# Performance work log

Hardware: AMD Instinct MI355X
Metric: run time of the kernel (lower is better)

Reference implementation:

```python
import jax, jax.numpy as jnp
import numpy as np

NUM_NODES = 116
EMBED = 64
HIDDEN = 64
OUT_FEAT = 116


def mish(x):
    return x * jnp.tanh(jax.nn.softplus(x))


def sage_conv(x, src, dst, w_l, b_l, w_r, n):
    # PyG SAGEConv (mean aggr): out = lin_l(mean_{j->i} x_j) + lin_r(x_i)
    agg = jax.ops.segment_sum(x[src], dst, num_segments=n)
    cnt = jax.ops.segment_sum(jnp.ones((src.shape[0],), x.dtype), dst, num_segments=n)
    mean = agg / jnp.clip(cnt, 1.0)[:, None]
    return mean @ w_l.T + b_l + x @ w_r.T


def setup_inputs() -> dict:
    key = jax.random.key(0)
    ks = jax.random.split(key, 12)
    B = 64
    N = B * NUM_NODES          # 7424 total nodes
    E = N * 32                 # 237568 edges
    d_in = EMBED * NUM_NODES   # 7424
    d_hid = HIDDEN * NUM_NODES # 7424
    d_out = OUT_FEAT * NUM_NODES  # 13456

    def lin_w(k, fan_out, fan_in):
        s = 1.0 / np.sqrt(fan_in)
        return jax.random.uniform(k, (fan_out, fan_in), jnp.float32, -s, s)

    return {
        "z": jax.random.normal(ks[0], (N, EMBED), jnp.float32),
        "edge_index": jax.random.randint(ks[1], (2, E), 0, N, jnp.int64),
        "batch_size": B,
        "w1_l": lin_w(ks[2], EMBED, EMBED),
        "b1_l": jnp.zeros((EMBED,), jnp.float32),
        "w1_r": lin_w(ks[3], EMBED, EMBED),
        "w2_l": lin_w(ks[4], EMBED, EMBED),
        "b2_l": jnp.zeros((EMBED,), jnp.float32),
        "w2_r": lin_w(ks[5], EMBED, EMBED),
        "fc1_w": lin_w(ks[6], d_hid, d_in),
        "fc1_b": jax.random.uniform(ks[7], (d_hid,), jnp.float32, -1/np.sqrt(d_in), 1/np.sqrt(d_in)),
        "fc2_w": lin_w(ks[8], d_out, d_hid),
        "fc2_b": jax.random.uniform(ks[9], (d_out,), jnp.float32, -1/np.sqrt(d_hid), 1/np.sqrt(d_hid)),
    }


def reference(z, edge_index, batch_size, w1_l, b1_l, w1_r, w2_l, b2_l, w2_r,
              fc1_w, fc1_b, fc2_w, fc2_b):
    n = z.shape[0]
    src, dst = edge_index[0], edge_index[1]
    h = mish(sage_conv(z, src, dst, w1_l, b1_l, w1_r, n))
    h = mish(sage_conv(h, src, dst, w2_l, b2_l, w2_r, n))
    h_flat = h.reshape(batch_size, NUM_NODES * EMBED)
    hidden = mish(h_flat @ fc1_w.T + fc1_b)
    x_rec = (hidden @ fc2_w.T + fc2_b).reshape(batch_size, NUM_NODES, OUT_FEAT)
    # enforce symmetry, unit diagonal
    sym = 0.5 * (x_rec + jnp.swapaxes(x_rec, 1, 2))
    eye = jnp.eye(NUM_NODES, dtype=bool)[None]
    sym = jnp.where(eye, jnp.asarray(1.0, sym.dtype), sym)
    return sym.reshape(batch_size * NUM_NODES, OUT_FEAT)
```

## Files before the change

### kernel.cpp

```cpp
#include <hip/hip_runtime.h>
#include <math.h>

#define NODES_TOT 7424
#define EDGES     237568
#define BATCH     64
#define NN        116
#define KDIM      7424
#define N1        7424
#define N2        13456
#define NKB       116
#define KSPLIT1   16
#define KSPLIT2   8

typedef __attribute__((ext_vector_type(8))) short bf16x8;
typedef __attribute__((ext_vector_type(4))) float f32x4;
typedef __attribute__((ext_vector_type(4))) short s16x4;

__device__ __forceinline__ float mish_f(float v) {
    float sp = fmaxf(v, 0.0f) + log1pf(expf(-fabsf(v)));
    return v * tanhf(sp);
}

__device__ __forceinline__ unsigned short bf_rne(float f) {
    unsigned u = __float_as_uint(f);
    u += 0x7fffu + ((u >> 16) & 1u);
    return (unsigned short)(u >> 16);
}

__global__ void zero_kernel(int* __restrict__ p, int n) {
    int i = blockIdx.x * 256 + threadIdx.x;
    if (i < n) p[i] = 0;
}

__global__ void hist_kernel(const int* __restrict__ dst, int* __restrict__ hist) {
    int e = blockIdx.x * 256 + threadIdx.x;
    if (e < EDGES) atomicAdd(&hist[dst[e]], 1);
}

__global__ void scan_kernel(const int* __restrict__ hist, int* __restrict__ row_start,
                            int* __restrict__ cursor) {
    __shared__ int s[1024];
    int t = threadIdx.x;
    int base = t * 8;
    int loc[8];
    int sum = 0;
    #pragma unroll
    for (int c = 0; c < 8; ++c) {
        int idx = base + c;
        int v = (idx < NODES_TOT) ? hist[idx] : 0;
        loc[c] = sum;
        sum += v;
    }
    s[t] = sum;
    __syncthreads();
    for (int off = 1; off < 1024; off <<= 1) {
        int v = (t >= off) ? s[t - off] : 0;
        __syncthreads();
        s[t] += v;
        __syncthreads();
    }
    int excl = s[t] - sum;
    #pragma unroll
    for (int c = 0; c < 8; ++c) {
        int idx = base + c;
        if (idx < NODES_TOT) {
            int r = excl + loc[c];
            row_start[idx] = r;
            cursor[idx] = r;
        }
    }
}

__global__ void csr_fill_kernel(const int* __restrict__ src, const int* __restrict__ dst,
                                int* __restrict__ cursor, int* __restrict__ csr_src) {
    int e = blockIdx.x * 256 + threadIdx.x;
    if (e < EDGES) {
        int p = atomicAdd(&cursor[dst[e]], 1);
        csr_src[p] = src[e];
    }
}

template <bool BF>
__global__ void __launch_bounds__(256) conv_kernel(
        const float* __restrict__ x, const int* __restrict__ csr_src,
        const int* __restrict__ row_start, const int* __restrict__ deg_arr,
        const float* __restrict__ w_l, const float* __restrict__ b_l,
        const float* __restrict__ w_r, void* __restrict__ h_out_v) {
    __shared__ float wlT[64 * 64];
    __shared__ float wrT[64 * 64];
    __shared__ float mv[4][64];
    __shared__ float xv[4][64];
    int t = threadIdx.x;
    for (int i = 0; i < 16; ++i) {
        int idx = t + i * 256;
        int f = idx >> 6, k = idx & 63;
        wlT[k * 64 + f] = w_l[idx];
        wrT[k * 64 + f] = w_r[idx];
    }
    int g = t >> 6, f = t & 63;
    __syncthreads();
    for (int nb = blockIdx.x * 4; nb < NODES_TOT; nb += gridDim.x * 4) {
        int node = nb + g;
        int deg = deg_arr[node];
        int rs = row_start[node];
        float sum = 0.f;
        for (int e = 0; e < deg; ++e) {
            int s = csr_src[rs + e];
            sum += x[s * 64 + f];
        }
        float mean = sum / (float)max(deg, 1);
        mv[g][f] = mean;
        xv[g][f] = x[node * 64 + f];
        __syncthreads();
        float o = b_l[f];
        #pragma unroll
        for (int k = 0; k < 64; ++k) {
            o = fmaf(mv[g][k], wlT[k * 64 + f], o);
            o = fmaf(xv[g][k], wrT[k * 64 + f], o);
        }
        float m = mish_f(o);
        if (BF) ((unsigned short*)h_out_v)[node * 64 + f] = bf_rne(m);
        else    ((float*)h_out_v)[node * 64 + f] = m;
        __syncthreads();
    }
}

template <int KSHIFT>
__global__ void __launch_bounds__(256) gemm_tile(
        const unsigned short* __restrict__ Abf, const float* __restrict__ W,
        float* __restrict__ Cp, int N) {
    __shared__ __align__(16) short Wsh[512 * 8];
    int t = threadIdx.x;
    int bx = blockIdx.x, by = blockIdx.y;
    int kb0 = (by * NKB) >> KSHIFT;
    int kb1 = ((by + 1) * NKB) >> KSHIFT;
    int n0 = bx * 64;
    int r = t >> 2, q = t & 3;
    int wr = n0 + r; if (wr >= N) wr = N - 1;
    const float* wsrc = W + (size_t)wr * KDIM + q * 4;
    int half = q & 1;
    int fbase = q >> 1;
    int wv = t >> 6, l = t & 63, l15 = l & 15, hi = l >> 4;
    f32x4 acc[4];
    #pragma unroll
    for (int g = 0; g < 4; ++g) acc[g] = (f32x4){0.f, 0.f, 0.f, 0.f};

    f32x4 w[4];
    {
        size_t k0 = (size_t)kb0 * 64;
        #pragma unroll
        for (int i = 0; i < 4; ++i) w[i] = *(const f32x4*)(wsrc + k0 + i * 16);
    }
    for (int kb = kb0; kb < kb1; ++kb) {
        s16x4 cv[4];
        #pragma unroll
        for (int i = 0; i < 4; ++i)
            #pragma unroll
            for (int j = 0; j < 4; ++j) cv[i][j] = (short)bf_rne(w[i][j]);
        __syncthreads();
        #pragma unroll
        for (int i = 0; i < 4; ++i)
            *(s16x4*)&Wsh[((i * 2 + fbase) * 64 + r) * 8 + half * 4] = cv[i];
        __syncthreads();
        if (kb + 1 < kb1) {
            size_t kn = (size_t)(kb + 1) * 64;
            #pragma unroll
            for (int i = 0; i < 4; ++i) w[i] = *(const f32x4*)(wsrc + kn + i * 16);
        }
        size_t k0 = (size_t)kb * 64;
        #pragma unroll
        for (int s = 0; s < 2; ++s) {
            int fw = s * 4 + hi;
            bf16x8 bh = *(const bf16x8*)&Wsh[(fw * 64 + wv * 16 + l15) * 8];
            #pragma unroll
            for (int g = 0; g < 4; ++g) {
                bf16x8 av = *(const bf16x8*)(Abf + (size_t)(g * 16 + l15) * KDIM + k0 + fw * 8);
                acc[g] = __builtin_amdgcn_mfma_f32_16x16x32_bf16(av, bh, acc[g], 0, 0, 0);
            }
        }
    }
    int gn = n0 + wv * 16 + l15;
    if (gn < N) {
        float* cp = Cp + (size_t)by * 64 * N;
        #pragma unroll
        for (int g = 0; g < 4; ++g)
            #pragma unroll
            for (int rr = 0; rr < 4; ++rr)
                cp[(size_t)(g * 16 + hi * 4 + rr) * N + gn] = acc[g][rr];
    }
}

__global__ void reduce1_kernel(const float* __restrict__ Cp, const float* __restrict__ b,
                               unsigned short* __restrict__ A2) {
    int i4 = (blockIdx.x * 256 + threadIdx.x) * 4;
    if (i4 >= BATCH * N1) return;
    int n = i4 % N1;
    f32x4 acc = *(const f32x4*)(b + n);
    #pragma unroll
    for (int s = 0; s < KSPLIT1; ++s)
        acc += *(const f32x4*)(Cp + (size_t)s * BATCH * N1 + i4);
    s16x4 o;
    #pragma unroll
    for (int j = 0; j < 4; ++j) o[j] = (short)bf_rne(mish_f(acc[j]));
    *(s16x4*)(A2 + i4) = o;
}

__global__ void reduce2_kernel(const float* __restrict__ Cp, const float* __restrict__ b,
                               float* __restrict__ C2) {
    int i4 = (blockIdx.x * 256 + threadIdx.x) * 4;
    if (i4 >= BATCH * N2) return;
    int n = i4 % N2;
    f32x4 acc = *(const f32x4*)(b + n);
    #pragma unroll
    for (int s = 0; s < KSPLIT2; ++s)
        acc += *(const f32x4*)(Cp + (size_t)s * BATCH * N2 + i4);
    *(f32x4*)(C2 + i4) = acc;
}

__global__ void sym_kernel(const float* __restrict__ C2, float* __restrict__ out) {
    int tid = blockIdx.x * 256 + threadIdx.x;
    if (tid >= BATCH * NN * NN) return;
    int j = tid % NN;
    int r = tid / NN;
    int i = r % NN;
    int b = r / NN;
    float v;
    if (i == j) {
        v = 1.0f;
    } else {
        v = 0.5f * (C2[(size_t)b * N2 + i * NN + j] + C2[(size_t)b * N2 + j * NN + i]);
    }
    out[tid] = v;
}

extern "C" void kernel_launch(void* const* d_in, const int* in_sizes, int n_in,
                              void* d_out, int out_size, void* d_ws, size_t ws_size,
                              hipStream_t stream) {
    const float* z     = (const float*)d_in[0];
    const int*   edge  = (const int*)d_in[1];
    const float* w1_l  = (const float*)d_in[3];
    const float* b1_l  = (const float*)d_in[4];
    const float* w1_r  = (const float*)d_in[5];
    const float* w2_l  = (const float*)d_in[6];
    const float* b2_l  = (const float*)d_in[7];
    const float* w2_r  = (const float*)d_in[8];
    const float* fc1_w = (const float*)d_in[9];
    const float* fc1_b = (const float*)d_in[10];
    const float* fc2_w = (const float*)d_in[11];
    const float* fc2_b = (const float*)d_in[12];
    float* out = (float*)d_out;

    char* ws = (char*)d_ws;
    size_t off = 0;
    auto alloc = [&](size_t bytes) {
        void* p = ws + off;
        off = (off + bytes + 255) & ~(size_t)255;
        return p;
    };
    int*            hist      = (int*)alloc(NODES_TOT * 4);
    int*            row_start = (int*)alloc(NODES_TOT * 4);
    int*            cursor    = (int*)alloc(NODES_TOT * 4);
    int*            csr_src   = (int*)alloc((size_t)EDGES * 4);
    float*          h1        = (float*)alloc((size_t)NODES_TOT * 64 * 4);
    unsigned short* A1        = (unsigned short*)alloc((size_t)NODES_TOT * 64 * 2);
    float*          Cp1       = (float*)alloc((size_t)KSPLIT1 * BATCH * N1 * 4);
    unsigned short* A2        = (unsigned short*)alloc((size_t)BATCH * N1 * 2);
    float*          Cp2       = (float*)alloc((size_t)KSPLIT2 * BATCH * N2 * 4);
    float*          C2        = (float*)alloc((size_t)BATCH * N2 * 4);

    const int* src = edge;
    const int* dst = edge + EDGES;

    zero_kernel<<<(NODES_TOT + 255) / 256, 256, 0, stream>>>(hist, NODES_TOT);
    hist_kernel<<<(EDGES + 255) / 256, 256, 0, stream>>>(dst, hist);
    scan_kernel<<<1, 1024, 0, stream>>>(hist, row_start, cursor);
    csr_fill_kernel<<<(EDGES + 255) / 256, 256, 0, stream>>>(src, dst, cursor, csr_src);

    conv_kernel<false><<<928, 256, 0, stream>>>(z, csr_src, row_start, hist, w1_l, b1_l, w1_r, h1);
    conv_kernel<true><<<928, 256, 0, stream>>>(h1, csr_src, row_start, hist, w2_l, b2_l, w2_r, A1);

    gemm_tile<4><<<dim3(N1 / 64, KSPLIT1), 256, 0, stream>>>(A1, fc1_w, Cp1, N1);
    reduce1_kernel<<<(BATCH * N1 / 4 + 255) / 256, 256, 0, stream>>>(Cp1, fc1_b, A2);

    gemm_tile<3><<<dim3((N2 + 63) / 64, KSPLIT2), 256, 0, stream>>>(A2, fc2_w, Cp2, N2);
    reduce2_kernel<<<(BATCH * N2 / 4 + 255) / 256, 256, 0, stream>>>(Cp2, fc2_b, C2);

    sym_kernel<<<(BATCH * NN * NN + 255) / 256, 256, 0, stream>>>(C2, out);
}
```

Measured before the change: 390.4 us.

## Replace split-K GEMM plus reduce kernels with in-block K-split deep GEMM

Each block now computes 16 output columns over the full K dimension, with the four waves each handling a quarter of K. The partial sums are reduced through shared memory and the bias (plus mish for fc1) is applied in the epilogue. This removes the large fp32 partial buffers and the separate reduce kernels, along with their global traffic. Loads are software-pipelined and LDS layouts are XOR-swizzled. The cost is that each block rereads all of A, grid sizes are smaller (464 and 841 blocks), and register pressure is high.

```diff
diff --git a/kernel.cpp b/kernel.cpp
--- a/kernel.cpp
+++ b/kernel.cpp
@@ -8,9 +8,8 @@
 #define KDIM      7424
 #define N1        7424
 #define N2        13456
-#define NKB       116
-#define KSPLIT1   16
-#define KSPLIT2   8
+#define KQ        1856
+#define NSUB      29
 
 typedef __attribute__((ext_vector_type(8))) short bf16x8;
 typedef __attribute__((ext_vector_type(4))) float f32x4;
@@ -125,96 +124,149 @@
     }
 }
 
-template <int KSHIFT>
-__global__ void __launch_bounds__(256) gemm_tile(
+template <bool MISH>
+__global__ void __launch_bounds__(256, 2) gemm_deep(
         const unsigned short* __restrict__ Abf, const float* __restrict__ W,
-        float* __restrict__ Cp, int N) {
-    __shared__ __align__(16) short Wsh[512 * 8];
+        const float* __restrict__ bias, void* __restrict__ Cout, int N) {
+    __shared__ __align__(16) unsigned short WP[4][16][32][8];
+    __shared__ __align__(16) unsigned short AB[4][64][8][8];
     int t = threadIdx.x;
-    int bx = blockIdx.x, by = blockIdx.y;
-    int kb0 = (by * NKB) >> KSHIFT;
-    int kb1 = ((by + 1) * NKB) >> KSHIFT;
-    int n0 = bx * 64;
-    int r = t >> 2, q = t & 3;
-    int wr = n0 + r; if (wr >= N) wr = N - 1;
-    const float* wsrc = W + (size_t)wr * KDIM + q * 4;
-    int half = q & 1;
-    int fbase = q >> 1;
     int wv = t >> 6, l = t & 63, l15 = l & 15, hi = l >> 4;
+    int n0 = blockIdx.x * 16;
+    size_t q0 = (size_t)wv * KQ;
+
+    const float* wbase = W + (size_t)n0 * KDIM + q0 + (size_t)l * 4;
+    const unsigned short* abase = Abf + q0 + (size_t)(l & 7) * 8;
+    int ar8 = l >> 3;
+
     f32x4 acc[4];
     #pragma unroll
     for (int g = 0; g < 4; ++g) acc[g] = (f32x4){0.f, 0.f, 0.f, 0.f};
 
-    f32x4 w[4];
+    f32x4 w[16];
+    f32x4 wt[4];
+    bf16x8 aN[8];
+
+#define IW(m) do {                                                         \
+        _Pragma("unroll")                                                  \
+        for (int j = 0; j < 16; ++j)                                       \
+            w[j] = *(const f32x4*)(wbase + (size_t)j * KDIM + (size_t)(m) * 256); \
+        __builtin_amdgcn_sched_barrier(0);                                 \
+    } while (0)
+
+#define IWT() do {                                                         \
+        _Pragma("unroll")                                                  \
+        for (int i = 0; i < 4; ++i)                                        \
+            wt[i] = *(const f32x4*)(W + (size_t)(n0 + i * 4 + hi) * KDIM + \
+                                    q0 + 1792 + (size_t)l15 * 4);          \
+        __builtin_amdgcn_sched_barrier(0);                                 \
+    } while (0)
+
+#define CW() do {                                                          \
+        _Pragma("unroll")                                                  \
+        for (int j = 0; j < 16; ++j) {                                     \
+            s16x4 cv;                                                      \
+            _Pragma("unroll")                                              \
+            for (int e = 0; e < 4; ++e) cv[e] = (short)bf_rne(w[j][e]);    \
+            *(s16x4*)&WP[wv][j][(l >> 1) ^ ((j & 7) << 2)][(l & 1) * 4] = cv; \
+        }                                                                  \
+    } while (0)
+
+#define CWT() do {                                                         \
+        _Pragma("unroll")                                                  \
+        for (int i = 0; i < 4; ++i) {                                      \
+            s16x4 cv;                                                      \
+            _Pragma("unroll")                                              \
+            for (int e = 0; e < 4; ++e) cv[e] = (short)bf_rne(wt[i][e]);   \
+            int r = i * 4 + hi;                                            \
+            *(s16x4*)&WP[wv][r][(l15 >> 1) ^ ((r & 7) << 2)][(l & 1) * 4] = cv; \
+        }                                                                  \
+    } while (0)
+
+#define IA(sg) do {                                                        \
+        _Pragma("unroll")                                                  \
+        for (int i = 0; i < 8; ++i)                                        \
+            aN[i] = *(const bf16x8*)(abase + (size_t)(i * 8 + ar8) * KDIM + \
+                                     (size_t)(sg) * 64);                   \
+    } while (0)
+
+#define DA() do {                                                          \
+        _Pragma("unroll")                                                  \
+        for (int i = 0; i < 8; ++i) {                                      \
+            int rr = i * 8 + ar8;                                          \
+            *(bf16x8*)&AB[wv][rr][(l & 7) ^ (rr & 7)][0] = aN[i];          \
+        }                                                                  \
+    } while (0)
+
+#define MFMAS(s) do {                                                      \
+        _Pragma("unroll")                                                  \
+        for (int u = 0; u < 2; ++u) {                                      \
+            int fw = u * 4 + hi;                                           \
+            bf16x8 bh = *(const bf16x8*)&WP[wv][l15][((s) * 8 + fw) ^ ((l15 & 7) << 2)][0]; \
+            _Pragma("unroll")                                              \
+            for (int g = 0; g < 4; ++g) {                                  \
+                int arr = g * 16 + l15;                                    \
+                bf16x8 avv = *(const bf16x8*)&AB[wv][arr][fw ^ (arr & 7)][0]; \
+                acc[g] = __builtin_amdgcn_mfma_f32_16x16x32_bf16(avv, bh, acc[g], 0, 0, 0); \
+            }                                                              \
+        }                                                                  \
+    } while (0)
+
+    IW(0);
+    IA(0);
+    CW();
+    DA();
+    IA(1);
+
+    for (int m = 0; m < 7; ++m) {
+        if (m < 6) IW(m + 1); else IWT();
+        #pragma unroll
+        for (int s = 0; s < 4; ++s) {
+            int sg = m * 4 + s;
+            MFMAS(s);
+            DA();
+            if (sg + 2 <= 28) IA(sg + 2);
+        }
+        if (m < 6) CW(); else CWT();
+    }
+    MFMAS(0);
+
+#undef IW
+#undef IWT
+#undef CW
+#undef CWT
+#undef IA
+#undef DA
+#undef MFMAS
+
+    __syncthreads();
+    float* CS = (float*)&WP[0][0][0][0];
+    #pragma unroll
+    for (int g = 0; g < 4; ++g)
+        #pragma unroll
+        for (int rr = 0; rr < 4; ++rr) {
+            int row = g * 16 + hi * 4 + rr;
+            CS[wv * 1024 + row * 16 + l15] = acc[g][rr];
+        }
+    __syncthreads();
     {
-        size_t k0 = (size_t)kb0 * 64;
-        #pragma unroll
-        for (int i = 0; i < 4; ++i) w[i] = *(const f32x4*)(wsrc + k0 + i * 16);
-    }
-    for (int kb = kb0; kb < kb1; ++kb) {
-        s16x4 cv[4];
-        #pragma unroll
-        for (int i = 0; i < 4; ++i)
+        int row = t >> 2;
+        int c0 = (t & 3) * 4;
+        f32x4 sum = *(const f32x4*)&CS[0 * 1024 + row * 16 + c0];
+        sum += *(const f32x4*)&CS[1 * 1024 + row * 16 + c0];
+        sum += *(const f32x4*)&CS[2 * 1024 + row * 16 + c0];
+        sum += *(const f32x4*)&CS[3 * 1024 + row * 16 + c0];
+        f32x4 b4 = *(const f32x4*)&bias[n0 + c0];
+        if (MISH) {
+            s16x4 o;
             #pragma unroll
-            for (int j = 0; j < 4; ++j) cv[i][j] = (short)bf_rne(w[i][j]);
-        __syncthreads();
-        #pragma unroll
-        for (int i = 0; i < 4; ++i)
-            *(s16x4*)&Wsh[((i * 2 + fbase) * 64 + r) * 8 + half * 4] = cv[i];
-        __syncthreads();
-        if (kb + 1 < kb1) {
-            size_t kn = (size_t)(kb + 1) * 64;
-            #pragma unroll
-            for (int i = 0; i < 4; ++i) w[i] = *(const f32x4*)(wsrc + kn + i * 16);
-        }
-        size_t k0 = (size_t)kb * 64;
-        #pragma unroll
-        for (int s = 0; s < 2; ++s) {
-            int fw = s * 4 + hi;
-            bf16x8 bh = *(const bf16x8*)&Wsh[(fw * 64 + wv * 16 + l15) * 8];
-            #pragma unroll
-            for (int g = 0; g < 4; ++g) {
-                bf16x8 av = *(const bf16x8*)(Abf + (size_t)(g * 16 + l15) * KDIM + k0 + fw * 8);
-                acc[g] = __builtin_amdgcn_mfma_f32_16x16x32_bf16(av, bh, acc[g], 0, 0, 0);
-            }
-        }
-    }
-    int gn = n0 + wv * 16 + l15;
-    if (gn < N) {
-        float* cp = Cp + (size_t)by * 64 * N;
-        #pragma unroll
-        for (int g = 0; g < 4; ++g)
-            #pragma unroll
-            for (int rr = 0; rr < 4; ++rr)
-                cp[(size_t)(g * 16 + hi * 4 + rr) * N + gn] = acc[g][rr];
-    }
-}
-
-__global__ void reduce1_kernel(const float* __restrict__ Cp, const float* __restrict__ b,
-                               unsigned short* __restrict__ A2) {
-    int i4 = (blockIdx.x * 256 + threadIdx.x) * 4;
-    if (i4 >= BATCH * N1) return;
-    int n = i4 % N1;
-    f32x4 acc = *(const f32x4*)(b + n);
-    #pragma unroll
-    for (int s = 0; s < KSPLIT1; ++s)
-        acc += *(const f32x4*)(Cp + (size_t)s * BATCH * N1 + i4);
-    s16x4 o;
-    #pragma unroll
-    for (int j = 0; j < 4; ++j) o[j] = (short)bf_rne(mish_f(acc[j]));
-    *(s16x4*)(A2 + i4) = o;
-}
-
-__global__ void reduce2_kernel(const float* __restrict__ Cp, const float* __restrict__ b,
-                               float* __restrict__ C2) {
-    int i4 = (blockIdx.x * 256 + threadIdx.x) * 4;
-    if (i4 >= BATCH * N2) return;
-    int n = i4 % N2;
-    f32x4 acc = *(const f32x4*)(b + n);
-    #pragma unroll
-    for (int s = 0; s < KSPLIT2; ++s)
-        acc += *(const f32x4*)(Cp + (size_t)s * BATCH * N2 + i4);
-    *(f32x4*)(C2 + i4) = acc;
+            for (int j = 0; j < 4; ++j) o[j] = (short)bf_rne(mish_f(sum[j] + b4[j]));
+            *(s16x4*)&((unsigned short*)Cout)[(size_t)row * N + n0 + c0] = o;
+        } else {
+            f32x4 o = sum + b4;
+            *(f32x4*)&((float*)Cout)[(size_t)row * N + n0 + c0] = o;
+        }
+    }
 }
 
 __global__ void sym_kernel(const float* __restrict__ C2, float* __restrict__ out) {
@@ -263,9 +315,7 @@
     int*            csr_src   = (int*)alloc((size_t)EDGES * 4);
     float*          h1        = (float*)alloc((size_t)NODES_TOT * 64 * 4);
     unsigned short* A1        = (unsigned short*)alloc((size_t)NODES_TOT * 64 * 2);
-    float*          Cp1       = (float*)alloc((size_t)KSPLIT1 * BATCH * N1 * 4);
     unsigned short* A2        = (unsigned short*)alloc((size_t)BATCH * N1 * 2);
-    float*          Cp2       = (float*)alloc((size_t)KSPLIT2 * BATCH * N2 * 4);
     float*          C2        = (float*)alloc((size_t)BATCH * N2 * 4);
 
     const int* src = edge;
@@ -279,11 +329,9 @@
     conv_kernel<false><<<928, 256, 0, stream>>>(z, csr_src, row_start, hist, w1_l, b1_l, w1_r, h1);
     conv_kernel<true><<<928, 256, 0, stream>>>(h1, csr_src, row_start, hist, w2_l, b2_l, w2_r, A1);
 
-    gemm_tile<4><<<dim3(N1 / 64, KSPLIT1), 256, 0, stream>>>(A1, fc1_w, Cp1, N1);
-    reduce1_kernel<<<(BATCH * N1 / 4 + 255) / 256, 256, 0, stream>>>(Cp1, fc1_b, A2);
-
-    gemm_tile<3><<<dim3((N2 + 63) / 64, KSPLIT2), 256, 0, stream>>>(A2, fc2_w, Cp2, N2);
-    reduce2_kernel<<<(BATCH * N2 / 4 + 255) / 256, 256, 0, stream>>>(Cp2, fc2_b, C2);
+    gemm_deep<true><<<N1 / 16, 256, 0, stream>>>(A1, fc1_w, fc1_b, A2, N1);
+
+    gemm_deep<false><<<N2 / 16, 256, 0, stream>>>(A2, fc2_w, fc2_b, C2, N2);
 
     sym_kernel<<<(BATCH * NN * NN + 255) / 256, 256, 0, stream>>>(C2, out);
 }
```

Result: faster. 339.1 us (-13.1%).
